# Kernel tuning notes

Hardware: AMD Instinct MI355X
Metric: run time of the kernel (lower is better)

The kernel has to match this reference:

```python
import jax, jax.numpy as jnp
import numpy as np

EPS = 1.0    # Lennard-Jones well depth
SIGMA = 1.0  # Lennard-Jones length scale


def setup_inputs() -> dict:
    key = jax.random.key(0)
    k1, k2, k3, k4 = jax.random.split(key, 4)
    B, N, D = 2, 4096, 3
    q = jax.random.normal(k1, (B, N, D), dtype=jnp.float32)
    p = jax.random.normal(k2, (B, N, D), dtype=jnp.float32)
    # masses strictly positive, away from zero
    m = jax.random.uniform(k3, (B, N, 1), dtype=jnp.float32, minval=0.5, maxval=1.5)
    t = jax.random.uniform(k4, (), dtype=jnp.float32)
    return {"q": q, "p": p, "m": m, "t": t}


def _lj_pair_force(q):
    # disp[b,i,j,:] = q[b,i,:] - q[b,j,:]   (torch: unsqueeze(-2) - unsqueeze(-3))
    disp = q[..., :, None, :] - q[..., None, :, :]          # [B,N,N,3]
    r2 = jnp.sum(disp * disp, axis=-1)                      # [B,N,N]
    mask = r2 > 0.0                                          # excludes i==j diagonal
    safe_r2 = jnp.where(mask, r2, 1.0)
    inv_r2 = jnp.where(mask, 1.0 / safe_r2, 0.0)
    s2 = (SIGMA * SIGMA) * inv_r2
    s6 = s2 * s2 * s2
    # LJ force on i from j: 24*eps*(2*s12 - s6)/r^2 * disp
    coeff = 24.0 * EPS * inv_r2 * s6 * (2.0 * s6 - 1.0)      # [B,N,N]
    force = coeff[..., None] * disp                          # [B,N,N,3]
    # sum(axis=-2): sum over partner index j
    return jnp.sum(force, axis=-2)                           # [B,N,3]


def reference(q, p, m, t):
    dq = p / m                   # Experiment.dq
    dp = _lj_pair_force(q)       # BasePairPotential.dp with LJ force
    return (dq, dp)
```

## Files before the change

### kernel.cpp

```cpp
#include <hip/hip_runtime.h>

#define BATCH    2
#define NPART    4096
#define NTHREADS 512
#define ILANES   2
#define IBLK     8
#define JCH      (NTHREADS / ILANES)
#define JLEN     (NPART / JCH)
#define NIB      (NPART / IBLK)
#define RSTRIDE  25

typedef float v2f __attribute__((ext_vector_type(2)));

template <bool MASKED>
__device__ inline void lj_pair(float jx, float jy, float jz,
                               v2f qx, v2f qy, v2f qz,
                               v2f& fx, v2f& fy, v2f& fz) {
    const v2f dx = qx - (v2f)jx;
    const v2f dy = qy - (v2f)jy;
    const v2f dz = qz - (v2f)jz;
    v2f r2 = dx * dx;
    r2 = __builtin_elementwise_fma(dy, dy, r2);
    r2 = __builtin_elementwise_fma(dz, dz, r2);
    v2f inv;
    if (MASKED) {
        inv.x = (r2.x > 0.0f) ? __builtin_amdgcn_rcpf(r2.x) : 0.0f;
        inv.y = (r2.y > 0.0f) ? __builtin_amdgcn_rcpf(r2.y) : 0.0f;
    } else {
        inv.x = __builtin_amdgcn_rcpf(r2.x);
        inv.y = __builtin_amdgcn_rcpf(r2.y);
    }
    const v2f inv2 = inv * inv;
    const v2f s6 = inv2 * inv;
    const v2f c1 = __builtin_elementwise_fma((v2f)48.0f, s6, (v2f)(-24.0f));
    const v2f coeff = (inv * s6) * c1;
    fx = __builtin_elementwise_fma(coeff, dx, fx);
    fy = __builtin_elementwise_fma(coeff, dy, fy);
    fz = __builtin_elementwise_fma(coeff, dz, fz);
}

template <bool MASKED>
__device__ inline void chunk_loop(const float4* __restrict__ jq4,
                                  v2f qx0, v2f qy0, v2f qz0,
                                  v2f qx1, v2f qy1, v2f qz1,
                                  v2f& fx0, v2f& fy0, v2f& fz0,
                                  v2f& fx1, v2f& fy1, v2f& fz1) {
    #pragma unroll
    for (int it = 0; it < JLEN / 4; ++it) {
        const float4 A = jq4[3 * it + 0];
        const float4 B = jq4[3 * it + 1];
        const float4 C = jq4[3 * it + 2];
        lj_pair<MASKED>(A.x, A.y, A.z, qx0, qy0, qz0, fx0, fy0, fz0);
        lj_pair<MASKED>(A.x, A.y, A.z, qx1, qy1, qz1, fx1, fy1, fz1);
        lj_pair<MASKED>(A.w, B.x, B.y, qx0, qy0, qz0, fx0, fy0, fz0);
        lj_pair<MASKED>(A.w, B.x, B.y, qx1, qy1, qz1, fx1, fy1, fz1);
        lj_pair<MASKED>(B.z, B.w, C.x, qx0, qy0, qz0, fx0, fy0, fz0);
        lj_pair<MASKED>(B.z, B.w, C.x, qx1, qy1, qz1, fx1, fy1, fz1);
        lj_pair<MASKED>(C.y, C.z, C.w, qx0, qy0, qz0, fx0, fy0, fz0);
        lj_pair<MASKED>(C.y, C.z, C.w, qx1, qy1, qz1, fx1, fy1, fz1);
    }
}

__global__ __launch_bounds__(NTHREADS, 4) void lj_fused(
        const float* __restrict__ q, const float* __restrict__ p,
        const float* __restrict__ m, float* __restrict__ dq,
        float* __restrict__ dp) {
    __shared__ float red[JCH * RSTRIDE];
    __shared__ float red2[24 * 16];

    const int ib = blockIdx.x;
    const int b  = blockIdx.y;
    const int t  = threadIdx.x;
    const int il = t & 1;
    const int jc = t >> 1;

    const float* qb = q + (size_t)b * NPART * 3;

    const int iA0 = ib * IBLK + il;
    const int iB0 = iA0 + 4;
    const int iA1 = iA0 + 2;
    const int iB1 = iA1 + 4;
    const v2f qx0 = {qb[iA0 * 3 + 0], qb[iB0 * 3 + 0]};
    const v2f qy0 = {qb[iA0 * 3 + 1], qb[iB0 * 3 + 1]};
    const v2f qz0 = {qb[iA0 * 3 + 2], qb[iB0 * 3 + 2]};
    const v2f qx1 = {qb[iA1 * 3 + 0], qb[iB1 * 3 + 0]};
    const v2f qy1 = {qb[iA1 * 3 + 1], qb[iB1 * 3 + 1]};
    const v2f qz1 = {qb[iA1 * 3 + 2], qb[iB1 * 3 + 2]};

    v2f fx0 = (v2f)0.0f, fy0 = (v2f)0.0f, fz0 = (v2f)0.0f;
    v2f fx1 = (v2f)0.0f, fy1 = (v2f)0.0f, fz1 = (v2f)0.0f;

    const float4* jq4 = (const float4*)(qb + (size_t)jc * JLEN * 3);

    if ((t >> 6) == (ib >> 6)) {
        chunk_loop<true >(jq4, qx0, qy0, qz0, qx1, qy1, qz1,
                          fx0, fy0, fz0, fx1, fy1, fz1);
    } else {
        chunk_loop<false>(jq4, qx0, qy0, qz0, qx1, qy1, qz1,
                          fx0, fy0, fz0, fx1, fy1, fz1);
    }

    {
        float* r = &red[jc * RSTRIDE + il];
        r[0]  = fx0.x;  r[2]  = fx0.y;  r[4]  = fx1.x;  r[6]  = fx1.y;
        r[8]  = fy0.x;  r[10] = fy0.y;  r[12] = fy1.x;  r[14] = fy1.y;
        r[16] = fz0.x;  r[18] = fz0.y;  r[20] = fz1.x;  r[22] = fz1.y;
    }
    __syncthreads();

    if (t < 384) {
        const int o  = t >> 4;
        const int g  = t & 15;
        const int comp = o >> 3;
        const int rr   = o & 7;
        const int il2  = rr & 1;
        const int cc2  = (rr >> 1) & 1;
        const int h2   = rr >> 2;
        const int slot = comp * 4 + cc2 * 2 + h2;
        float s = 0.0f;
        #pragma unroll
        for (int qq = 0; qq < 16; ++qq) {
            s += red[(g * 16 + qq) * RSTRIDE + slot * 2 + il2];
        }
        red2[o * 16 + g] = s;
    }
    __syncthreads();

    if (t < 24) {
        float s = 0.0f;
        #pragma unroll
        for (int g = 0; g < 16; ++g) s += red2[t * 16 + g];
        const int comp = t >> 3;
        const int ii   = t & 7;
        const size_t gi = (size_t)b * NPART + ib * IBLK + ii;
        dp[gi * 3 + comp] = s;
        dq[gi * 3 + comp] = p[gi * 3 + comp] / m[gi];
    }
}

extern "C" void kernel_launch(void* const* d_in, const int* in_sizes, int n_in,
                              void* d_out, int out_size, void* d_ws, size_t ws_size,
                              hipStream_t stream) {
    const float* q = (const float*)d_in[0];
    const float* p = (const float*)d_in[1];
    const float* m = (const float*)d_in[2];

    const int n_elem = BATCH * NPART * 3;
    float* dq_out = (float*)d_out;
    float* dp_out = (float*)d_out + n_elem;

    dim3 grid(NIB, BATCH);
    lj_fused<<<grid, NTHREADS, 0, stream>>>(q, p, m, dq_out, dp_out);
}
```

Baseline: 18.61 us.

## Shrink blocks to 256 threads with 4 i-particles each

Each block now handles 4 i-particles with 256 threads, and every thread walks a j-chunk of 16 particles, down from 512 threads covering 8 particles in 2 lanes. The grid doubles to 1024x2 blocks and launch bounds now ask for 8 blocks per CU. The shared-memory reduction is simplified and the masked-chunk test is updated to match. The aim is finer-grained scheduling and a smaller reduction per block, at the cost of more blocks and the same j-data being reloaded by twice as many blocks.

```diff
diff --git a/kernel.cpp b/kernel.cpp
--- a/kernel.cpp
+++ b/kernel.cpp
@@ -2,13 +2,12 @@
 
 #define BATCH    2
 #define NPART    4096
-#define NTHREADS 512
-#define ILANES   2
-#define IBLK     8
-#define JCH      (NTHREADS / ILANES)
+#define NTHREADS 256
+#define IBLK     4
+#define JCH      NTHREADS
 #define JLEN     (NPART / JCH)
 #define NIB      (NPART / IBLK)
-#define RSTRIDE  25
+#define RSTRIDE  13
 
 typedef float v2f __attribute__((ext_vector_type(2)));
 
@@ -61,38 +60,33 @@
     }
 }
 
-__global__ __launch_bounds__(NTHREADS, 4) void lj_fused(
+__global__ __launch_bounds__(NTHREADS, 8) void lj_fused(
         const float* __restrict__ q, const float* __restrict__ p,
         const float* __restrict__ m, float* __restrict__ dq,
         float* __restrict__ dp) {
     __shared__ float red[JCH * RSTRIDE];
-    __shared__ float red2[24 * 16];
+    __shared__ float red2[12 * 16];
 
     const int ib = blockIdx.x;
     const int b  = blockIdx.y;
     const int t  = threadIdx.x;
-    const int il = t & 1;
-    const int jc = t >> 1;
 
     const float* qb = q + (size_t)b * NPART * 3;
+    const int ibase = ib * IBLK;
 
-    const int iA0 = ib * IBLK + il;
-    const int iB0 = iA0 + 4;
-    const int iA1 = iA0 + 2;
-    const int iB1 = iA1 + 4;
-    const v2f qx0 = {qb[iA0 * 3 + 0], qb[iB0 * 3 + 0]};
-    const v2f qy0 = {qb[iA0 * 3 + 1], qb[iB0 * 3 + 1]};
-    const v2f qz0 = {qb[iA0 * 3 + 2], qb[iB0 * 3 + 2]};
-    const v2f qx1 = {qb[iA1 * 3 + 0], qb[iB1 * 3 + 0]};
-    const v2f qy1 = {qb[iA1 * 3 + 1], qb[iB1 * 3 + 1]};
-    const v2f qz1 = {qb[iA1 * 3 + 2], qb[iB1 * 3 + 2]};
+    const v2f qx0 = {qb[(ibase + 0) * 3 + 0], qb[(ibase + 1) * 3 + 0]};
+    const v2f qy0 = {qb[(ibase + 0) * 3 + 1], qb[(ibase + 1) * 3 + 1]};
+    const v2f qz0 = {qb[(ibase + 0) * 3 + 2], qb[(ibase + 1) * 3 + 2]};
+    const v2f qx1 = {qb[(ibase + 2) * 3 + 0], qb[(ibase + 3) * 3 + 0]};
+    const v2f qy1 = {qb[(ibase + 2) * 3 + 1], qb[(ibase + 3) * 3 + 1]};
+    const v2f qz1 = {qb[(ibase + 2) * 3 + 2], qb[(ibase + 3) * 3 + 2]};
 
     v2f fx0 = (v2f)0.0f, fy0 = (v2f)0.0f, fz0 = (v2f)0.0f;
     v2f fx1 = (v2f)0.0f, fy1 = (v2f)0.0f, fz1 = (v2f)0.0f;
 
-    const float4* jq4 = (const float4*)(qb + (size_t)jc * JLEN * 3);
+    const float4* jq4 = (const float4*)(qb + (size_t)t * JLEN * 3);
 
-    if ((t >> 6) == (ib >> 6)) {
+    if ((t >> 6) == (ib >> 8)) {
         chunk_loop<true >(jq4, qx0, qy0, qz0, qx1, qy1, qz1,
                           fx0, fy0, fz0, fx1, fy1, fz1);
     } else {
@@ -101,38 +95,32 @@
     }
 
     {
-        float* r = &red[jc * RSTRIDE + il];
-        r[0]  = fx0.x;  r[2]  = fx0.y;  r[4]  = fx1.x;  r[6]  = fx1.y;
-        r[8]  = fy0.x;  r[10] = fy0.y;  r[12] = fy1.x;  r[14] = fy1.y;
-        r[16] = fz0.x;  r[18] = fz0.y;  r[20] = fz1.x;  r[22] = fz1.y;
+        float* r = &red[t * RSTRIDE];
+        r[0]  = fx0.x;  r[1]  = fx0.y;  r[2]  = fx1.x;  r[3]  = fx1.y;
+        r[4]  = fy0.x;  r[5]  = fy0.y;  r[6]  = fy1.x;  r[7]  = fy1.y;
+        r[8]  = fz0.x;  r[9]  = fz0.y;  r[10] = fz1.x;  r[11] = fz1.y;
     }
     __syncthreads();
 
-    if (t < 384) {
-        const int o  = t >> 4;
-        const int g  = t & 15;
-        const int comp = o >> 3;
-        const int rr   = o & 7;
-        const int il2  = rr & 1;
-        const int cc2  = (rr >> 1) & 1;
-        const int h2   = rr >> 2;
-        const int slot = comp * 4 + cc2 * 2 + h2;
+    if (t < 192) {
+        const int o = t >> 4;
+        const int g = t & 15;
         float s = 0.0f;
         #pragma unroll
         for (int qq = 0; qq < 16; ++qq) {
-            s += red[(g * 16 + qq) * RSTRIDE + slot * 2 + il2];
+            s += red[(qq * 16 + g) * RSTRIDE + o];
         }
         red2[o * 16 + g] = s;
     }
     __syncthreads();
 
-    if (t < 24) {
+    if (t < 12) {
         float s = 0.0f;
         #pragma unroll
         for (int g = 0; g < 16; ++g) s += red2[t * 16 + g];
-        const int comp = t >> 3;
-        const int ii   = t & 7;
-        const size_t gi = (size_t)b * NPART + ib * IBLK + ii;
+        const int comp = t >> 2;
+        const int ii   = t & 3;
+        const size_t gi = (size_t)b * NPART + ibase + ii;
         dp[gi * 3 + comp] = s;
         dq[gi * 3 + comp] = p[gi * 3 + comp] / m[gi];
     }
```

Result: slower. 19.28 us (+3.6%).
